# Kernel tuning notes

Hardware: AMD Instinct MI355X
Metric: run time of the kernel (lower is better)

Reference implementation:

```python
import jax, jax.numpy as jnp
import numpy as np

B = 16          # number of trees (batch)
H = 256         # hidden_size == feature_size
S = 16          # Tree.num_sem
C = 5           # max_child_num (complete C-ary tree)
L = 6           # tree depth: leaves at level L, internal levels 0..L-1
N_LEAF = C**L                     # 15625
N_INT = (C**L - 1) // (C - 1)     # 3906 internal nodes, level-l offset = (C^l-1)/(C-1)


def setup_inputs() -> dict:
    key = jax.random.key(0)
    ks = jax.random.split(key, 20)
    rn = lambda k, shp, s=0.05: jax.random.normal(k, shp, dtype=jnp.float32) * s
    return {
        "leaf_box": jax.random.normal(ks[0], (B, N_LEAF, 4), dtype=jnp.float32),
        "leaf_sem": jax.random.uniform(ks[1], (B, N_LEAF, S), dtype=jnp.float32),
        "internal_box": jax.random.normal(ks[2], (B, N_INT, 4), dtype=jnp.float32),
        "node_type": jax.random.randint(ks[3], (B, N_INT), 0, 3, dtype=jnp.int32),
        "eps": jax.random.normal(ks[4], (B, H), dtype=jnp.float32),
        "W_box": rn(ks[5], (4, H)), "b_box": jnp.zeros((H,), jnp.float32),
        "W_sem": rn(ks[6], (S, H)), "b_sem": jnp.zeros((H,), jnp.float32),
        "W_node": rn(ks[7], (3, C * H, H)), "b_node": jnp.zeros((3, H), jnp.float32),
        "W1": rn(ks[8], (H, H)), "b1": jnp.zeros((H,), jnp.float32),
        "Wmu": rn(ks[9], (H, H)), "bmu": jnp.zeros((H,), jnp.float32),
        "Wvar": rn(ks[10], (H, H)), "bvar": jnp.zeros((H,), jnp.float32),
    }


def reference(leaf_box, leaf_sem, internal_box, node_type, eps,
              W_box, b_box, W_sem, b_sem, W_node, b_node,
              W1, b1, Wmu, bmu, Wvar, bvar):
    box_enc = lambda b: jax.nn.relu(b @ W_box + b_box)
    # LeafEncoder: relu-box-encoding + relu-sem-encoding
    feats = box_enc(leaf_box) + jax.nn.relu(leaf_sem @ W_sem + b_sem)  # [B, N_LEAF, H]
    # Bottom-up over internal levels (static loop over L=6 levels)
    for l in range(L - 1, -1, -1):
        n = C ** l
        off = (C ** l - 1) // (C - 1)
        child = feats.reshape(B, n, C * H)  # children flattened per parent (child_exists==1)
        # Apply all 3 branch encoders (vertical/horizontal/stack), select by node label
        y_all = jnp.einsum('bnk,tkh->bnth', child, W_node) + b_node          # [B,n,3,H]
        sel = jax.nn.one_hot(node_type[:, off:off + n], 3, dtype=child.dtype)  # [B,n,3]
        y = jnp.einsum('bnth,bnt->bnh', y_all, sel)
        feats = jax.nn.relu(y) + box_enc(internal_box[:, off:off + n])
    root = feats[:, 0]  # [B, H]
    # Sampler (variational, probabilistic)
    enc = jax.nn.relu(root @ W1 + b1)
    mu = enc @ Wmu + bmu
    logvar = enc @ Wvar + bvar
    std = jnp.exp(0.5 * logvar)
    kld = 1.0 + logvar - mu ** 2 - jnp.exp(logvar)
    return jnp.concatenate([eps * std + mu, kld], axis=1)  # [B, 2H]
```

## Files before the change

kernel.cpp:

```cpp
#include <hip/hip_runtime.h>


#define B_ 16
#define H_ 256
#define NLEAF 15625
#define NINT 3906

typedef __bf16 bf16_t;
typedef bf16_t bf16x8 __attribute__((ext_vector_type(8)));
typedef bf16_t bf16x4 __attribute__((ext_vector_type(4)));
typedef float f32x4 __attribute__((ext_vector_type(4)));

__device__ __forceinline__ void gl2lds16(const bf16_t* g, bf16_t* l) {
  __builtin_amdgcn_global_load_lds((const __attribute__((address_space(1))) void*)g,
                                   (__attribute__((address_space(3))) void*)l,
                                   16, 0, 0);
}

__global__ __launch_bounds__(256) void prep_kernel(const float* __restrict__ W_node,
                                                   bf16_t* __restrict__ Wt,
                                                   int* __restrict__ counters) {
  if (blockIdx.x == 0 && threadIdx.x < 18) counters[threadIdx.x] = 0;
  const int t = blockIdx.x / 80;
  const int kc = blockIdx.x % 80;
  const int h = threadIdx.x;
  const float* srcp = W_node + (size_t)t * 1280 * 256 + h;
  bf16_t* dstp = Wt + ((size_t)(t * 256 + h)) * 1280;
#pragma unroll
  for (int k0 = kc * 16; k0 < kc * 16 + 16; k0 += 8) {
    bf16x8 v;
#pragma unroll
    for (int j = 0; j < 8; ++j) v[j] = (bf16_t)srcp[(size_t)(k0 + j) * 256];
    *(bf16x8*)(dstp + k0) = v;
  }
}

__global__ __launch_bounds__(256) void leaf_kernel(
    const float* __restrict__ leaf_box, const float* __restrict__ leaf_sem,
    const float* __restrict__ W_box, const float* __restrict__ b_box,
    const float* __restrict__ W_sem, const float* __restrict__ b_sem,
    bf16_t* __restrict__ f6) {
  const int lane = threadIdx.x & 63;
  const int wave = threadIdx.x >> 6;
  const int h0 = lane * 4;
  float wb[4][4], ws[16][4], bb[4], bs[4];
#pragma unroll
  for (int j = 0; j < 4; ++j) {
    float4 v = *(const float4*)(W_box + j * H_ + h0);
    wb[j][0] = v.x; wb[j][1] = v.y; wb[j][2] = v.z; wb[j][3] = v.w;
  }
#pragma unroll
  for (int j = 0; j < 16; ++j) {
    float4 v = *(const float4*)(W_sem + j * H_ + h0);
    ws[j][0] = v.x; ws[j][1] = v.y; ws[j][2] = v.z; ws[j][3] = v.w;
  }
  {
    float4 v = *(const float4*)(b_box + h0);
    bb[0] = v.x; bb[1] = v.y; bb[2] = v.z; bb[3] = v.w;
    float4 u = *(const float4*)(b_sem + h0);
    bs[0] = u.x; bs[1] = u.y; bs[2] = u.z; bs[3] = u.w;
  }
  const int ROWS = B_ * NLEAF;
  const int stride = gridDim.x * 4;
  for (int row = blockIdx.x * 4 + wave; row < ROWS; row += stride) {
    float4 bx = *(const float4*)(leaf_box + (size_t)row * 4);
    const float4* sp = (const float4*)(leaf_sem + (size_t)row * 16);
    float4 sv0 = sp[0], sv1 = sp[1], sv2 = sp[2], sv3 = sp[3];
    bf16x4 o;
#pragma unroll
    for (int c = 0; c < 4; ++c) {
      float s1 = fmaf(wb[0][c], bx.x, fmaf(wb[1][c], bx.y,
                 fmaf(wb[2][c], bx.z, fmaf(wb[3][c], bx.w, bb[c]))));
      float s2 = bs[c];
      s2 = fmaf(ws[0][c], sv0.x, s2);  s2 = fmaf(ws[1][c], sv0.y, s2);
      s2 = fmaf(ws[2][c], sv0.z, s2);  s2 = fmaf(ws[3][c], sv0.w, s2);
      s2 = fmaf(ws[4][c], sv1.x, s2);  s2 = fmaf(ws[5][c], sv1.y, s2);
      s2 = fmaf(ws[6][c], sv1.z, s2);  s2 = fmaf(ws[7][c], sv1.w, s2);
      s2 = fmaf(ws[8][c], sv2.x, s2);  s2 = fmaf(ws[9][c], sv2.y, s2);
      s2 = fmaf(ws[10][c], sv2.z, s2); s2 = fmaf(ws[11][c], sv2.w, s2);
      s2 = fmaf(ws[12][c], sv3.x, s2); s2 = fmaf(ws[13][c], sv3.y, s2);
      s2 = fmaf(ws[14][c], sv3.z, s2); s2 = fmaf(ws[15][c], sv3.w, s2);
      o[c] = (bf16_t)(fmaxf(s1, 0.f) + fmaxf(s2, 0.f));
    }
    *(bf16x4*)(f6 + (size_t)row * H_ + h0) = o;
  }
}

__global__ __launch_bounds__(256) void bucket_kernel(const int* __restrict__ node_type,
                                                     int* __restrict__ counters,
                                                     int2* __restrict__ buckets) {
  __shared__ int lcnt[18];
  __shared__ int lbase[18];
  const int tid = threadIdx.x;
  if (tid < 18) lcnt[tid] = 0;
  __syncthreads();

  int idx = blockIdx.x * 256 + tid;
  bool active = idx < B_ * NINT;
  int t = 0, key = 0, mypos = 0;
  int2 e;
  int base = 0, nl_cap = 0;
  if (active) {
    int b = idx / NINT;
    int j = idx - b * NINT;
    int l, off;
    if (j >= 781)      { l = 5; off = 781; }
    else if (j >= 156) { l = 4; off = 156; }
    else if (j >= 31)  { l = 3; off = 31; }
    else if (j >= 6)   { l = 2; off = 6; }
    else if (j >= 1)   { l = 1; off = 1; }
    else               { l = 0; off = 0; }
    const int n_tab[6]    = {1, 5, 25, 125, 625, 3125};
    const int nn_tab[6]   = {5, 25, 125, 625, 3125, 15625};
    const int base_tab[6] = {0, 48, 288, 1488, 7488, 37488};
    int n_l = n_tab[l], nn = nn_tab[l];
    t = node_type[idx];
    int i = j - off;
    e.x = b * n_l + i;
    e.y = b * nn + 5 * i;
    base = base_tab[l];
    nl_cap = B_ * n_l;
    key = l * 3 + t;
    mypos = atomicAdd(&lcnt[key], 1);
  }
  __syncthreads();
  if (tid < 18) {
    int c = lcnt[tid];
    lbase[tid] = c ? atomicAdd(&counters[tid], c) : 0;
  }
  __syncthreads();
  if (active) {
    buckets[base + t * nl_cap + lbase[key] + mypos] = e;
  }
}

__global__ __launch_bounds__(256) void level_kernel(
    const bf16_t* __restrict__ src, bf16_t* __restrict__ dst,
    const int2* __restrict__ bucket, const int* __restrict__ counters,
    const bf16_t* __restrict__ Wt, const float* __restrict__ b_node,
    const float* __restrict__ ibox, const float* __restrict__ W_box,
    const float* __restrict__ b_box, int n_l, int off_l, int cap) {
  const int t = blockIdx.y;
  const int cnt = counters[t];
  const int tile0 = blockIdx.x * 128;
  if (tile0 >= cnt) return;
  const int nblk = blockIdx.z;
  const int2* rd = bucket + (size_t)t * cap;

  __shared__ __align__(16) bf16_t Asm[2][128][64];
  __shared__ __align__(16) bf16_t Bsm[2][128][64];

  const int tid = threadIdx.x;
  const int lane = tid & 63;
  const int wave = tid >> 6;
  const int wm = wave & 1, wn = wave >> 1;
  const int quad = lane >> 4;
  const int l15 = lane & 15;

  const int r8 = tid >> 3;
  const int sc = tid & 7;
  const bf16_t* wsrc = Wt + ((size_t)t * 256 + nblk * 128) * 1280;
  const bf16_t* aptr[4];
  const bf16_t* bptr[4];
#pragma unroll
  for (int i = 0; i < 4; ++i) {
    int r = i * 32 + r8;
    int gch = sc ^ ((r >> 1) & 7);
    int ai = tile0 + r;
    if (ai >= cnt) ai = cnt - 1;
    aptr[i] = src + (size_t)rd[ai].y * H_ + gch * 8;
    bptr[i] = wsrc + (size_t)r * 1280 + gch * 8;
  }

  f32x4 acc[4][4];
#pragma unroll
  for (int i = 0; i < 4; ++i)
#pragma unroll
    for (int j = 0; j < 4; ++j) acc[i][j] = (f32x4){0.f, 0.f, 0.f, 0.f};

  const int sw = (l15 >> 1) & 7;
  const int pc0 = ((0 * 4 + quad) ^ sw) * 8;
  const int pc1 = ((1 * 4 + quad) ^ sw) * 8;

#define STAGE(buf, ks)                                          \
  {                                                             \
    const int ko = (ks) * 64;                                   \
    bf16_t* la = &Asm[buf][0][0] + wave * 512;                  \
    bf16_t* lb = &Bsm[buf][0][0] + wave * 512;                  \
    _Pragma("unroll") for (int i = 0; i < 4; ++i)               \
        gl2lds16(aptr[i] + ko, la + i * 2048);                  \
    _Pragma("unroll") for (int i = 0; i < 4; ++i)               \
        gl2lds16(bptr[i] + ko, lb + i * 2048);                  \
  }

  STAGE(0, 0)
  for (int ks = 0; ks < 20; ++ks) {
    const int buf = ks & 1;
    __syncthreads();
    bf16x8 af0[4], af1[4], bf0[4], bf1[4];
#pragma unroll
    for (int am = 0; am < 4; ++am) {
      af0[am] = *(const bf16x8*)(&Asm[buf][wm * 64 + am * 16 + l15][pc0]);
      af1[am] = *(const bf16x8*)(&Asm[buf][wm * 64 + am * 16 + l15][pc1]);
    }
#pragma unroll
    for (int bn = 0; bn < 4; ++bn) {
      bf0[bn] = *(const bf16x8*)(&Bsm[buf][wn * 64 + bn * 16 + l15][pc0]);
      bf1[bn] = *(const bf16x8*)(&Bsm[buf][wn * 64 + bn * 16 + l15][pc1]);
    }
    if (ks + 1 < 20) STAGE(buf ^ 1, ks + 1)
#pragma unroll
    for (int am = 0; am < 4; ++am)
#pragma unroll
      for (int bn = 0; bn < 4; ++bn)
        acc[am][bn] = __builtin_amdgcn_mfma_f32_16x16x32_bf16(af0[am], bf0[bn], acc[am][bn], 0, 0, 0);
#pragma unroll
    for (int am = 0; am < 4; ++am)
#pragma unroll
      for (int bn = 0; bn < 4; ++bn)
        acc[am][bn] = __builtin_amdgcn_mfma_f32_16x16x32_bf16(af1[am], bf1[bn], acc[am][bn], 0, 0, 0);
  }
#undef STAGE

  float wbv[4][6];
#pragma unroll
  for (int bn = 0; bn < 4; ++bn) {
    int col = nblk * 128 + wn * 64 + bn * 16 + l15;
    wbv[bn][0] = W_box[col];
    wbv[bn][1] = W_box[H_ + col];
    wbv[bn][2] = W_box[2 * H_ + col];
    wbv[bn][3] = W_box[3 * H_ + col];
    wbv[bn][4] = b_box[col];
    wbv[bn][5] = b_node[t * H_ + col];
  }
#pragma unroll
  for (int am = 0; am < 4; ++am) {
    int orow[4]; float4 bxv[4]; bool valid[4];
#pragma unroll
    for (int r = 0; r < 4; ++r) {
      int gidx = tile0 + wm * 64 + am * 16 + quad * 4 + r;
      valid[r] = (gidx < cnt);
      int ic = valid[r] ? gidx : (cnt - 1);
      int orw = rd[ic].x;
      orow[r] = orw;
      int b = orw / n_l;
      int i = orw - b * n_l;
      bxv[r] = *(const float4*)(ibox + ((size_t)b * NINT + off_l + i) * 4);
    }
#pragma unroll
    for (int bn = 0; bn < 4; ++bn) {
      int col = nblk * 128 + wn * 64 + bn * 16 + l15;
#pragma unroll
      for (int r = 0; r < 4; ++r) {
        if (!valid[r]) continue;
        float y = fmaxf(acc[am][bn][r] + wbv[bn][5], 0.f);
        float be = fmaf(wbv[bn][0], bxv[r].x,
                   fmaf(wbv[bn][1], bxv[r].y,
                   fmaf(wbv[bn][2], bxv[r].z,
                   fmaf(wbv[bn][3], bxv[r].w, wbv[bn][4]))));
        be = fmaxf(be, 0.f);
        dst[(size_t)orow[r] * H_ + col] = (bf16_t)(y + be);
      }
    }
  }
}

__global__ __launch_bounds__(256) void head_kernel(
    const bf16_t* __restrict__ f0, const float* __restrict__ eps,
    const float* __restrict__ W1, const float* __restrict__ b1,
    const float* __restrict__ Wmu, const float* __restrict__ bmu,
    const float* __restrict__ Wvar, const float* __restrict__ bvar,
    float* __restrict__ out) {
  __shared__ float root[256];
  __shared__ float enc[256];
  int b = blockIdx.x, h = threadIdx.x;
  root[h] = (float)f0[b * H_ + h];
  __syncthreads();
  float a = b1[h];
  for (int k = 0; k < 256; ++k) a = fmaf(root[k], W1[k * H_ + h], a);
  enc[h] = fmaxf(a, 0.f);
  __syncthreads();
  float m = bmu[h], lv = bvar[h];
  for (int k = 0; k < 256; ++k) {
    float e = enc[k];
    m = fmaf(e, Wmu[k * H_ + h], m);
    lv = fmaf(e, Wvar[k * H_ + h], lv);
  }
  float stdv = expf(0.5f * lv);
  float kld = 1.f + lv - m * m - expf(lv);
  out[b * 512 + h] = eps[b * H_ + h] * stdv + m;
  out[b * 512 + 256 + h] = kld;
}

extern "C" void kernel_launch(void* const* d_in, const int* in_sizes, int n_in,
                              void* d_out, int out_size, void* d_ws, size_t ws_size,
                              hipStream_t stream) {
  const float* leaf_box     = (const float*)d_in[0];
  const float* leaf_sem     = (const float*)d_in[1];
  const float* internal_box = (const float*)d_in[2];
  const int*   node_type    = (const int*)d_in[3];
  const float* eps          = (const float*)d_in[4];
  const float* W_box        = (const float*)d_in[5];
  const float* b_box        = (const float*)d_in[6];
  const float* W_sem        = (const float*)d_in[7];
  const float* b_sem        = (const float*)d_in[8];
  const float* W_node       = (const float*)d_in[9];
  const float* b_node       = (const float*)d_in[10];
  const float* W1           = (const float*)d_in[11];
  const float* b1           = (const float*)d_in[12];
  const float* Wmu          = (const float*)d_in[13];
  const float* bmu          = (const float*)d_in[14];
  const float* Wvar         = (const float*)d_in[15];
  const float* bvar         = (const float*)d_in[16];
  float* out = (float*)d_out;

  char* p = (char*)d_ws;
  auto alloc = [&](size_t bytes) {
    char* r = p;
    p += (bytes + 255) & ~(size_t)255;
    return r;
  };
  bf16_t* Wt = (bf16_t*)alloc((size_t)3 * 256 * 1280 * 2);
  const int n_tab[7] = {1, 5, 25, 125, 625, 3125, 15625};
  bf16_t* f[7];
  for (int l = 0; l <= 6; ++l) f[l] = (bf16_t*)alloc((size_t)B_ * n_tab[l] * H_ * 2);
  int* counters = (int*)alloc(18 * 4);
  int2* buckets = (int2*)alloc((size_t)187488 * 8);

  hipLaunchKernelGGL(prep_kernel, dim3(240), dim3(256), 0, stream, W_node, Wt, counters);
  hipLaunchKernelGGL(leaf_kernel, dim3(2048), dim3(256), 0, stream,
                     leaf_box, leaf_sem, W_box, b_box, W_sem, b_sem, f[6]);
  hipLaunchKernelGGL(bucket_kernel, dim3((B_ * NINT + 255) / 256), dim3(256), 0, stream,
                     node_type, counters, buckets);

  const int lvl_base[6] = {0, 48, 288, 1488, 7488, 37488};
  const int off_tab[6]  = {0, 1, 6, 31, 156, 781};
  for (int l = 5; l >= 0; --l) {
    int cap = B_ * n_tab[l];
    int tiles = (cap + 127) / 128;
    hipLaunchKernelGGL(level_kernel, dim3(tiles, 3, 2), dim3(256), 0, stream,
                       f[l + 1], f[l], buckets + lvl_base[l], counters + l * 3,
                       Wt, b_node, internal_box, W_box, b_box,
                       n_tab[l], off_tab[l], cap);
  }
  hipLaunchKernelGGL(head_kernel, dim3(16), dim3(256), 0, stream,
                     f[0], eps, W1, b1, Wmu, bmu, Wvar, bvar, out);
}
```

Measured before the change: 392.7 us.

## Scatter node features directly into type-sorted contiguous GEMM input rows

Producers (leaf kernel and each level kernel) now compute each parent's position in the type-bucketed order and write child features straight into a contiguous A matrix of 1280-wide rows. The level GEMM then reads its A operand as plain contiguous rows instead of gathering through bucket indices. This removes the indirect gather on the A loads and makes them fully sequential. In exchange the writes become scattered, and extra node_pos/node_type lookups are added in the epilogues. The head kernel also gets an unroll pragma.

```diff
diff --git a/kernel.cpp b/kernel.cpp
--- a/kernel.cpp
+++ b/kernel.cpp
@@ -35,60 +35,10 @@
   }
 }
 
-__global__ __launch_bounds__(256) void leaf_kernel(
-    const float* __restrict__ leaf_box, const float* __restrict__ leaf_sem,
-    const float* __restrict__ W_box, const float* __restrict__ b_box,
-    const float* __restrict__ W_sem, const float* __restrict__ b_sem,
-    bf16_t* __restrict__ f6) {
-  const int lane = threadIdx.x & 63;
-  const int wave = threadIdx.x >> 6;
-  const int h0 = lane * 4;
-  float wb[4][4], ws[16][4], bb[4], bs[4];
-#pragma unroll
-  for (int j = 0; j < 4; ++j) {
-    float4 v = *(const float4*)(W_box + j * H_ + h0);
-    wb[j][0] = v.x; wb[j][1] = v.y; wb[j][2] = v.z; wb[j][3] = v.w;
-  }
-#pragma unroll
-  for (int j = 0; j < 16; ++j) {
-    float4 v = *(const float4*)(W_sem + j * H_ + h0);
-    ws[j][0] = v.x; ws[j][1] = v.y; ws[j][2] = v.z; ws[j][3] = v.w;
-  }
-  {
-    float4 v = *(const float4*)(b_box + h0);
-    bb[0] = v.x; bb[1] = v.y; bb[2] = v.z; bb[3] = v.w;
-    float4 u = *(const float4*)(b_sem + h0);
-    bs[0] = u.x; bs[1] = u.y; bs[2] = u.z; bs[3] = u.w;
-  }
-  const int ROWS = B_ * NLEAF;
-  const int stride = gridDim.x * 4;
-  for (int row = blockIdx.x * 4 + wave; row < ROWS; row += stride) {
-    float4 bx = *(const float4*)(leaf_box + (size_t)row * 4);
-    const float4* sp = (const float4*)(leaf_sem + (size_t)row * 16);
-    float4 sv0 = sp[0], sv1 = sp[1], sv2 = sp[2], sv3 = sp[3];
-    bf16x4 o;
-#pragma unroll
-    for (int c = 0; c < 4; ++c) {
-      float s1 = fmaf(wb[0][c], bx.x, fmaf(wb[1][c], bx.y,
-                 fmaf(wb[2][c], bx.z, fmaf(wb[3][c], bx.w, bb[c]))));
-      float s2 = bs[c];
-      s2 = fmaf(ws[0][c], sv0.x, s2);  s2 = fmaf(ws[1][c], sv0.y, s2);
-      s2 = fmaf(ws[2][c], sv0.z, s2);  s2 = fmaf(ws[3][c], sv0.w, s2);
-      s2 = fmaf(ws[4][c], sv1.x, s2);  s2 = fmaf(ws[5][c], sv1.y, s2);
-      s2 = fmaf(ws[6][c], sv1.z, s2);  s2 = fmaf(ws[7][c], sv1.w, s2);
-      s2 = fmaf(ws[8][c], sv2.x, s2);  s2 = fmaf(ws[9][c], sv2.y, s2);
-      s2 = fmaf(ws[10][c], sv2.z, s2); s2 = fmaf(ws[11][c], sv2.w, s2);
-      s2 = fmaf(ws[12][c], sv3.x, s2); s2 = fmaf(ws[13][c], sv3.y, s2);
-      s2 = fmaf(ws[14][c], sv3.z, s2); s2 = fmaf(ws[15][c], sv3.w, s2);
-      o[c] = (bf16_t)(fmaxf(s1, 0.f) + fmaxf(s2, 0.f));
-    }
-    *(bf16x4*)(f6 + (size_t)row * H_ + h0) = o;
-  }
-}
-
 __global__ __launch_bounds__(256) void bucket_kernel(const int* __restrict__ node_type,
                                                      int* __restrict__ counters,
-                                                     int2* __restrict__ buckets) {
+                                                     int2* __restrict__ buckets,
+                                                     int* __restrict__ node_pos) {
   __shared__ int lcnt[18];
   __shared__ int lbase[18];
   const int tid = threadIdx.x;
@@ -110,14 +60,14 @@
     else if (j >= 6)   { l = 2; off = 6; }
     else if (j >= 1)   { l = 1; off = 1; }
     else               { l = 0; off = 0; }
-    const int n_tab[6]    = {1, 5, 25, 125, 625, 3125};
-    const int nn_tab[6]   = {5, 25, 125, 625, 3125, 15625};
-    const int base_tab[6] = {0, 48, 288, 1488, 7488, 37488};
-    int n_l = n_tab[l], nn = nn_tab[l];
+    const int n_tab[6]        = {1, 5, 25, 125, 625, 3125};
+    const int base_tab[6]     = {0, 48, 288, 1488, 7488, 37488};
+    const int off_prev_tab[6] = {0, 0, 1, 6, 31, 156};
+    int n_l = n_tab[l];
     t = node_type[idx];
     int i = j - off;
     e.x = b * n_l + i;
-    e.y = b * nn + 5 * i;
+    e.y = (l == 0) ? b : (b * NINT + off_prev_tab[l] + i / 5);
     base = base_tab[l];
     nl_cap = B_ * n_l;
     key = l * 3 + t;
@@ -130,20 +80,88 @@
   }
   __syncthreads();
   if (active) {
-    buckets[base + t * nl_cap + lbase[key] + mypos] = e;
+    int pos = lbase[key] + mypos;
+    buckets[base + t * nl_cap + pos] = e;
+    node_pos[idx] = pos;
+  }
+}
+
+__global__ __launch_bounds__(256) void leaf_kernel(
+    const float* __restrict__ leaf_box, const float* __restrict__ leaf_sem,
+    const float* __restrict__ W_box, const float* __restrict__ b_box,
+    const float* __restrict__ W_sem, const float* __restrict__ b_sem,
+    const int* __restrict__ node_type, const int* __restrict__ node_pos,
+    const int* __restrict__ counters5, bf16_t* __restrict__ A5) {
+  const int lane = threadIdx.x & 63;
+  const int wave = threadIdx.x >> 6;
+  const int h0 = lane * 4;
+  float wb[4][4], ws[16][4], bb[4], bs[4];
+#pragma unroll
+  for (int j = 0; j < 4; ++j) {
+    float4 v = *(const float4*)(W_box + j * H_ + h0);
+    wb[j][0] = v.x; wb[j][1] = v.y; wb[j][2] = v.z; wb[j][3] = v.w;
+  }
+#pragma unroll
+  for (int j = 0; j < 16; ++j) {
+    float4 v = *(const float4*)(W_sem + j * H_ + h0);
+    ws[j][0] = v.x; ws[j][1] = v.y; ws[j][2] = v.z; ws[j][3] = v.w;
+  }
+  {
+    float4 v = *(const float4*)(b_box + h0);
+    bb[0] = v.x; bb[1] = v.y; bb[2] = v.z; bb[3] = v.w;
+    float4 u = *(const float4*)(b_sem + h0);
+    bs[0] = u.x; bs[1] = u.y; bs[2] = u.z; bs[3] = u.w;
+  }
+  const int c15 = counters5[0], c16 = counters5[1];
+  const int GROUPS = B_ * 3125;
+  const int stride = gridDim.x * 4;
+  for (int g = blockIdx.x * 4 + wave; g < GROUPS; g += stride) {
+    int b = g / 3125;
+    int i = g - b * 3125;
+    int pidx = b * NINT + 781 + i;
+    int pt = node_type[pidx];
+    int gpos = node_pos[pidx] + (pt > 0 ? c15 : 0) + (pt > 1 ? c16 : 0);
+    size_t outbase = (size_t)gpos * 1280 + h0;
+    size_t leaf0 = (size_t)b * NLEAF + 5 * i;
+#pragma unroll
+    for (int c = 0; c < 5; ++c) {
+      float4 bx = *(const float4*)(leaf_box + (leaf0 + c) * 4);
+      const float4* sp = (const float4*)(leaf_sem + (leaf0 + c) * 16);
+      float4 sv0 = sp[0], sv1 = sp[1], sv2 = sp[2], sv3 = sp[3];
+      bf16x4 o;
+#pragma unroll
+      for (int ch = 0; ch < 4; ++ch) {
+        float s1 = fmaf(wb[0][ch], bx.x, fmaf(wb[1][ch], bx.y,
+                   fmaf(wb[2][ch], bx.z, fmaf(wb[3][ch], bx.w, bb[ch]))));
+        float s2 = bs[ch];
+        s2 = fmaf(ws[0][ch], sv0.x, s2);  s2 = fmaf(ws[1][ch], sv0.y, s2);
+        s2 = fmaf(ws[2][ch], sv0.z, s2);  s2 = fmaf(ws[3][ch], sv0.w, s2);
+        s2 = fmaf(ws[4][ch], sv1.x, s2);  s2 = fmaf(ws[5][ch], sv1.y, s2);
+        s2 = fmaf(ws[6][ch], sv1.z, s2);  s2 = fmaf(ws[7][ch], sv1.w, s2);
+        s2 = fmaf(ws[8][ch], sv2.x, s2);  s2 = fmaf(ws[9][ch], sv2.y, s2);
+        s2 = fmaf(ws[10][ch], sv2.z, s2); s2 = fmaf(ws[11][ch], sv2.w, s2);
+        s2 = fmaf(ws[12][ch], sv3.x, s2); s2 = fmaf(ws[13][ch], sv3.y, s2);
+        s2 = fmaf(ws[14][ch], sv3.z, s2); s2 = fmaf(ws[15][ch], sv3.w, s2);
+        o[ch] = (bf16_t)(fmaxf(s1, 0.f) + fmaxf(s2, 0.f));
+      }
+      *(bf16x4*)(A5 + outbase + c * 256) = o;
+    }
   }
 }
 
 __global__ __launch_bounds__(256) void level_kernel(
-    const bf16_t* __restrict__ src, bf16_t* __restrict__ dst,
+    const bf16_t* __restrict__ Ain, bf16_t* __restrict__ Aout,
     const int2* __restrict__ bucket, const int* __restrict__ counters,
+    const int* __restrict__ pcounters, const int* __restrict__ node_pos,
+    const int* __restrict__ node_type,
     const bf16_t* __restrict__ Wt, const float* __restrict__ b_node,
     const float* __restrict__ ibox, const float* __restrict__ W_box,
-    const float* __restrict__ b_box, int n_l, int off_l, int cap) {
+    const float* __restrict__ b_box, int n_l, int off_l, int cap, int is_root) {
   const int t = blockIdx.y;
   const int cnt = counters[t];
   const int tile0 = blockIdx.x * 128;
   if (tile0 >= cnt) return;
+  const int tbase = (t > 0 ? counters[0] : 0) + (t > 1 ? counters[1] : 0);
   const int nblk = blockIdx.z;
   const int2* rd = bucket + (size_t)t * cap;
 
@@ -166,9 +184,7 @@
   for (int i = 0; i < 4; ++i) {
     int r = i * 32 + r8;
     int gch = sc ^ ((r >> 1) & 7);
-    int ai = tile0 + r;
-    if (ai >= cnt) ai = cnt - 1;
-    aptr[i] = src + (size_t)rd[ai].y * H_ + gch * 8;
+    aptr[i] = Ain + (size_t)(tbase + tile0 + r) * 1280 + gch * 8;
     bptr[i] = wsrc + (size_t)r * 1280 + gch * 8;
   }
 
@@ -222,6 +238,7 @@
   }
 #undef STAGE
 
+  const int pc0v = pcounters[0], pc1v = pcounters[1];
   float wbv[4][6];
 #pragma unroll
   for (int bn = 0; bn < 4; ++bn) {
@@ -235,17 +252,28 @@
   }
 #pragma unroll
   for (int am = 0; am < 4; ++am) {
-    int orow[4]; float4 bxv[4]; bool valid[4];
+    size_t wofs[4]; float4 bxv[4]; bool valid[4];
 #pragma unroll
     for (int r = 0; r < 4; ++r) {
       int gidx = tile0 + wm * 64 + am * 16 + quad * 4 + r;
       valid[r] = (gidx < cnt);
       int ic = valid[r] ? gidx : (cnt - 1);
-      int orw = rd[ic].x;
-      orow[r] = orw;
-      int b = orw / n_l;
-      int i = orw - b * n_l;
+      int2 e = rd[ic];
+      int orow = e.x;
+      int b = orow / n_l;
+      int i = orow - b * n_l;
       bxv[r] = *(const float4*)(ibox + ((size_t)b * NINT + off_l + i) * 4);
+      int wtgt;
+      if (is_root) {
+        wtgt = orow;
+      } else {
+        int pidx = e.y;
+        int pt = node_type[pidx];
+        int gpos = node_pos[pidx] + (pt > 0 ? pc0v : 0) + (pt > 1 ? pc1v : 0);
+        int cs = i - (i / 5) * 5;
+        wtgt = gpos * 5 + cs;
+      }
+      wofs[r] = (size_t)wtgt * 256;
     }
 #pragma unroll
     for (int bn = 0; bn < 4; ++bn) {
@@ -259,7 +287,7 @@
                    fmaf(wbv[bn][2], bxv[r].z,
                    fmaf(wbv[bn][3], bxv[r].w, wbv[bn][4]))));
         be = fmaxf(be, 0.f);
-        dst[(size_t)orow[r] * H_ + col] = (bf16_t)(y + be);
+        Aout[wofs[r] + col] = (bf16_t)(y + be);
       }
     }
   }
@@ -277,10 +305,12 @@
   root[h] = (float)f0[b * H_ + h];
   __syncthreads();
   float a = b1[h];
+#pragma unroll 8
   for (int k = 0; k < 256; ++k) a = fmaf(root[k], W1[k * H_ + h], a);
   enc[h] = fmaxf(a, 0.f);
   __syncthreads();
   float m = bmu[h], lv = bvar[h];
+#pragma unroll 8
   for (int k = 0; k < 256; ++k) {
     float e = enc[k];
     m = fmaf(e, Wmu[k * H_ + h], m);
@@ -321,28 +351,35 @@
     return r;
   };
   bf16_t* Wt = (bf16_t*)alloc((size_t)3 * 256 * 1280 * 2);
-  const int n_tab[7] = {1, 5, 25, 125, 625, 3125, 15625};
-  bf16_t* f[7];
-  for (int l = 0; l <= 6; ++l) f[l] = (bf16_t*)alloc((size_t)B_ * n_tab[l] * H_ * 2);
+  const int n_nodes[6] = {1, 5, 25, 125, 625, 3125};
+  bf16_t* A[6];
+  for (int l = 0; l < 6; ++l)
+    A[l] = (bf16_t*)alloc(((size_t)B_ * n_nodes[l] + 128) * 1280 * 2);
+  bf16_t* f0 = (bf16_t*)alloc((size_t)B_ * H_ * 2);
   int* counters = (int*)alloc(18 * 4);
+  int* node_pos = (int*)alloc((size_t)B_ * NINT * 4);
   int2* buckets = (int2*)alloc((size_t)187488 * 8);
 
   hipLaunchKernelGGL(prep_kernel, dim3(240), dim3(256), 0, stream, W_node, Wt, counters);
+  hipLaunchKernelGGL(bucket_kernel, dim3((B_ * NINT + 255) / 256), dim3(256), 0, stream,
+                     node_type, counters, buckets, node_pos);
   hipLaunchKernelGGL(leaf_kernel, dim3(2048), dim3(256), 0, stream,
-                     leaf_box, leaf_sem, W_box, b_box, W_sem, b_sem, f[6]);
-  hipLaunchKernelGGL(bucket_kernel, dim3((B_ * NINT + 255) / 256), dim3(256), 0, stream,
-                     node_type, counters, buckets);
+                     leaf_box, leaf_sem, W_box, b_box, W_sem, b_sem,
+                     node_type, node_pos, counters + 15, A[5]);
 
   const int lvl_base[6] = {0, 48, 288, 1488, 7488, 37488};
   const int off_tab[6]  = {0, 1, 6, 31, 156, 781};
   for (int l = 5; l >= 0; --l) {
-    int cap = B_ * n_tab[l];
+    int cap = B_ * n_nodes[l];
     int tiles = (cap + 127) / 128;
+    bf16_t* Aout = (l > 0) ? A[l - 1] : f0;
+    const int* pctr = (l > 0) ? (counters + (l - 1) * 3) : counters;
     hipLaunchKernelGGL(level_kernel, dim3(tiles, 3, 2), dim3(256), 0, stream,
-                       f[l + 1], f[l], buckets + lvl_base[l], counters + l * 3,
+                       A[l], Aout, buckets + lvl_base[l], counters + l * 3, pctr,
+                       node_pos, node_type,
                        Wt, b_node, internal_box, W_box, b_box,
-                       n_tab[l], off_tab[l], cap);
+                       n_nodes[l], off_tab[l], cap, (l == 0) ? 1 : 0);
   }
   hipLaunchKernelGGL(head_kernel, dim3(16), dim3(256), 0, stream,
-                     f[0], eps, W1, b1, Wmu, bmu, Wvar, bvar, out);
-}
+                     f0, eps, W1, b1, Wmu, bmu, Wvar, bvar, out);
+}
```

Measured after the change: 438.8 us. 11.7% more time.

## Fuse upper tree levels and head into one persistent kernel with grid barriers

Applied to the files above, without the earlier changes.

Merges weight prep and bucketing into one launch, keeps level 5 as its own kernel, and runs levels 4..0 plus the VAE head in a single persistent 256-block kernel with atomic grid barriers between levels. It also unrolls the leaf kernel to four rows per wave. The goal is to remove the launch overhead and tail latency of the small upper levels, at the cost of spin-wait barriers that need all 256 blocks to be resident at once, and idle blocks on the tiny levels.

```diff
diff --git a/kernel.cpp b/kernel.cpp
--- a/kernel.cpp
+++ b/kernel.cpp
@@ -5,6 +5,7 @@
 #define H_ 256
 #define NLEAF 15625
 #define NINT 3906
+#define GPERS 256
 
 typedef __bf16 bf16_t;
 typedef bf16_t bf16x8 __attribute__((ext_vector_type(8)));
@@ -17,85 +18,30 @@
                                    16, 0, 0);
 }
 
-__global__ __launch_bounds__(256) void prep_kernel(const float* __restrict__ W_node,
-                                                   bf16_t* __restrict__ Wt,
-                                                   int* __restrict__ counters) {
-  if (blockIdx.x == 0 && threadIdx.x < 18) counters[threadIdx.x] = 0;
-  const int t = blockIdx.x / 80;
-  const int kc = blockIdx.x % 80;
-  const int h = threadIdx.x;
-  const float* srcp = W_node + (size_t)t * 1280 * 256 + h;
-  bf16_t* dstp = Wt + ((size_t)(t * 256 + h)) * 1280;
-#pragma unroll
-  for (int k0 = kc * 16; k0 < kc * 16 + 16; k0 += 8) {
-    bf16x8 v;
-#pragma unroll
-    for (int j = 0; j < 8; ++j) v[j] = (bf16_t)srcp[(size_t)(k0 + j) * 256];
-    *(bf16x8*)(dstp + k0) = v;
-  }
-}
-
-__global__ __launch_bounds__(256) void leaf_kernel(
-    const float* __restrict__ leaf_box, const float* __restrict__ leaf_sem,
-    const float* __restrict__ W_box, const float* __restrict__ b_box,
-    const float* __restrict__ W_sem, const float* __restrict__ b_sem,
-    bf16_t* __restrict__ f6) {
-  const int lane = threadIdx.x & 63;
-  const int wave = threadIdx.x >> 6;
-  const int h0 = lane * 4;
-  float wb[4][4], ws[16][4], bb[4], bs[4];
-#pragma unroll
-  for (int j = 0; j < 4; ++j) {
-    float4 v = *(const float4*)(W_box + j * H_ + h0);
-    wb[j][0] = v.x; wb[j][1] = v.y; wb[j][2] = v.z; wb[j][3] = v.w;
-  }
-#pragma unroll
-  for (int j = 0; j < 16; ++j) {
-    float4 v = *(const float4*)(W_sem + j * H_ + h0);
-    ws[j][0] = v.x; ws[j][1] = v.y; ws[j][2] = v.z; ws[j][3] = v.w;
-  }
-  {
-    float4 v = *(const float4*)(b_box + h0);
-    bb[0] = v.x; bb[1] = v.y; bb[2] = v.z; bb[3] = v.w;
-    float4 u = *(const float4*)(b_sem + h0);
-    bs[0] = u.x; bs[1] = u.y; bs[2] = u.z; bs[3] = u.w;
-  }
-  const int ROWS = B_ * NLEAF;
-  const int stride = gridDim.x * 4;
-  for (int row = blockIdx.x * 4 + wave; row < ROWS; row += stride) {
-    float4 bx = *(const float4*)(leaf_box + (size_t)row * 4);
-    const float4* sp = (const float4*)(leaf_sem + (size_t)row * 16);
-    float4 sv0 = sp[0], sv1 = sp[1], sv2 = sp[2], sv3 = sp[3];
-    bf16x4 o;
-#pragma unroll
-    for (int c = 0; c < 4; ++c) {
-      float s1 = fmaf(wb[0][c], bx.x, fmaf(wb[1][c], bx.y,
-                 fmaf(wb[2][c], bx.z, fmaf(wb[3][c], bx.w, bb[c]))));
-      float s2 = bs[c];
-      s2 = fmaf(ws[0][c], sv0.x, s2);  s2 = fmaf(ws[1][c], sv0.y, s2);
-      s2 = fmaf(ws[2][c], sv0.z, s2);  s2 = fmaf(ws[3][c], sv0.w, s2);
-      s2 = fmaf(ws[4][c], sv1.x, s2);  s2 = fmaf(ws[5][c], sv1.y, s2);
-      s2 = fmaf(ws[6][c], sv1.z, s2);  s2 = fmaf(ws[7][c], sv1.w, s2);
-      s2 = fmaf(ws[8][c], sv2.x, s2);  s2 = fmaf(ws[9][c], sv2.y, s2);
-      s2 = fmaf(ws[10][c], sv2.z, s2); s2 = fmaf(ws[11][c], sv2.w, s2);
-      s2 = fmaf(ws[12][c], sv3.x, s2); s2 = fmaf(ws[13][c], sv3.y, s2);
-      s2 = fmaf(ws[14][c], sv3.z, s2); s2 = fmaf(ws[15][c], sv3.w, s2);
-      o[c] = (bf16_t)(fmaxf(s1, 0.f) + fmaxf(s2, 0.f));
-    }
-    *(bf16x4*)(f6 + (size_t)row * H_ + h0) = o;
-  }
-}
-
-__global__ __launch_bounds__(256) void bucket_kernel(const int* __restrict__ node_type,
-                                                     int* __restrict__ counters,
-                                                     int2* __restrict__ buckets) {
+__global__ __launch_bounds__(256) void prep_bucket_kernel(
+    const float* __restrict__ W_node, bf16_t* __restrict__ Wt,
+    const int* __restrict__ node_type, int* __restrict__ counters,
+    int2* __restrict__ buckets) {
+  const int tid = threadIdx.x;
+  if (blockIdx.x < 240) {
+    const int t = blockIdx.x / 80;
+    const int kc = blockIdx.x % 80;
+    const float* srcp = W_node + (size_t)t * 1280 * 256 + tid;
+    bf16_t* dstp = Wt + ((size_t)(t * 256 + tid)) * 1280;
+#pragma unroll
+    for (int k0 = kc * 16; k0 < kc * 16 + 16; k0 += 8) {
+      bf16x8 v;
+#pragma unroll
+      for (int j = 0; j < 8; ++j) v[j] = (bf16_t)srcp[(size_t)(k0 + j) * 256];
+      *(bf16x8*)(dstp + k0) = v;
+    }
+    return;
+  }
   __shared__ int lcnt[18];
   __shared__ int lbase[18];
-  const int tid = threadIdx.x;
   if (tid < 18) lcnt[tid] = 0;
   __syncthreads();
-
-  int idx = blockIdx.x * 256 + tid;
+  int idx = (blockIdx.x - 240) * 256 + tid;
   bool active = idx < B_ * NINT;
   int t = 0, key = 0, mypos = 0;
   int2 e;
@@ -129,27 +75,73 @@
     lbase[tid] = c ? atomicAdd(&counters[tid], c) : 0;
   }
   __syncthreads();
-  if (active) {
-    buckets[base + t * nl_cap + lbase[key] + mypos] = e;
-  }
-}
-
-__global__ __launch_bounds__(256) void level_kernel(
+  if (active) buckets[base + t * nl_cap + lbase[key] + mypos] = e;
+}
+
+__global__ __launch_bounds__(256) void leaf_kernel(
+    const float* __restrict__ leaf_box, const float* __restrict__ leaf_sem,
+    const float* __restrict__ W_box, const float* __restrict__ b_box,
+    const float* __restrict__ W_sem, const float* __restrict__ b_sem,
+    bf16_t* __restrict__ f6) {
+  const int lane = threadIdx.x & 63;
+  const int wave = threadIdx.x >> 6;
+  const int h0 = lane * 4;
+  float wb[4][4], ws[16][4], bb[4], bs[4];
+#pragma unroll
+  for (int j = 0; j < 4; ++j) {
+    float4 v = *(const float4*)(W_box + j * H_ + h0);
+    wb[j][0] = v.x; wb[j][1] = v.y; wb[j][2] = v.z; wb[j][3] = v.w;
+  }
+#pragma unroll
+  for (int j = 0; j < 16; ++j) {
+    float4 v = *(const float4*)(W_sem + j * H_ + h0);
+    ws[j][0] = v.x; ws[j][1] = v.y; ws[j][2] = v.z; ws[j][3] = v.w;
+  }
+  {
+    float4 v = *(const float4*)(b_box + h0);
+    bb[0] = v.x; bb[1] = v.y; bb[2] = v.z; bb[3] = v.w;
+    float4 u = *(const float4*)(b_sem + h0);
+    bs[0] = u.x; bs[1] = u.y; bs[2] = u.z; bs[3] = u.w;
+  }
+  const int ROWS = B_ * NLEAF;
+  const int stride = gridDim.x * 16;
+  for (int row = blockIdx.x * 16 + wave * 4; row < ROWS; row += stride) {
+    float4 bx[4]; float4 sv[4][4];
+#pragma unroll
+    for (int r = 0; r < 4; ++r) {
+      bx[r] = *(const float4*)(leaf_box + (size_t)(row + r) * 4);
+      const float4* sp = (const float4*)(leaf_sem + (size_t)(row + r) * 16);
+      sv[r][0] = sp[0]; sv[r][1] = sp[1]; sv[r][2] = sp[2]; sv[r][3] = sp[3];
+    }
+#pragma unroll
+    for (int r = 0; r < 4; ++r) {
+      bf16x4 o;
+#pragma unroll
+      for (int c = 0; c < 4; ++c) {
+        float s1 = fmaf(wb[0][c], bx[r].x, fmaf(wb[1][c], bx[r].y,
+                   fmaf(wb[2][c], bx[r].z, fmaf(wb[3][c], bx[r].w, bb[c]))));
+        float s2 = bs[c];
+#pragma unroll
+        for (int j = 0; j < 4; ++j) {
+          s2 = fmaf(ws[4*j+0][c], sv[r][j].x, s2);
+          s2 = fmaf(ws[4*j+1][c], sv[r][j].y, s2);
+          s2 = fmaf(ws[4*j+2][c], sv[r][j].z, s2);
+          s2 = fmaf(ws[4*j+3][c], sv[r][j].w, s2);
+        }
+        o[c] = (bf16_t)(fmaxf(s1, 0.f) + fmaxf(s2, 0.f));
+      }
+      *(bf16x4*)(f6 + (size_t)(row + r) * H_ + h0) = o;
+    }
+  }
+}
+
+__device__ __forceinline__ void level_tile(
+    bf16_t* __restrict__ As, bf16_t* __restrict__ Bs,
     const bf16_t* __restrict__ src, bf16_t* __restrict__ dst,
-    const int2* __restrict__ bucket, const int* __restrict__ counters,
-    const bf16_t* __restrict__ Wt, const float* __restrict__ b_node,
+    const int2* __restrict__ rd, int cnt,
+    const bf16_t* __restrict__ wsrc, const float* __restrict__ b_node_t,
     const float* __restrict__ ibox, const float* __restrict__ W_box,
-    const float* __restrict__ b_box, int n_l, int off_l, int cap) {
-  const int t = blockIdx.y;
-  const int cnt = counters[t];
-  const int tile0 = blockIdx.x * 128;
-  if (tile0 >= cnt) return;
-  const int nblk = blockIdx.z;
-  const int2* rd = bucket + (size_t)t * cap;
-
-  __shared__ __align__(16) bf16_t Asm[2][128][64];
-  __shared__ __align__(16) bf16_t Bsm[2][128][64];
-
+    const float* __restrict__ b_box, int n_l, int off_l, int tile0, int nblk) {
   const int tid = threadIdx.x;
   const int lane = tid & 63;
   const int wave = tid >> 6;
@@ -159,7 +151,6 @@
 
   const int r8 = tid >> 3;
   const int sc = tid & 7;
-  const bf16_t* wsrc = Wt + ((size_t)t * 256 + nblk * 128) * 1280;
   const bf16_t* aptr[4];
   const bf16_t* bptr[4];
 #pragma unroll
@@ -179,18 +170,18 @@
     for (int j = 0; j < 4; ++j) acc[i][j] = (f32x4){0.f, 0.f, 0.f, 0.f};
 
   const int sw = (l15 >> 1) & 7;
-  const int pc0 = ((0 * 4 + quad) ^ sw) * 8;
-  const int pc1 = ((1 * 4 + quad) ^ sw) * 8;
-
-#define STAGE(buf, ks)                                          \
-  {                                                             \
-    const int ko = (ks) * 64;                                   \
-    bf16_t* la = &Asm[buf][0][0] + wave * 512;                  \
-    bf16_t* lb = &Bsm[buf][0][0] + wave * 512;                  \
-    _Pragma("unroll") for (int i = 0; i < 4; ++i)               \
-        gl2lds16(aptr[i] + ko, la + i * 2048);                  \
-    _Pragma("unroll") for (int i = 0; i < 4; ++i)               \
-        gl2lds16(bptr[i] + ko, lb + i * 2048);                  \
+  const int pc0 = (quad ^ sw) * 8;
+  const int pc1 = ((4 + quad) ^ sw) * 8;
+
+#define STAGE(buf, ks)                                            \
+  {                                                               \
+    const int ko = (ks) * 64;                                     \
+    bf16_t* la = As + (buf) * 8192 + wave * 512;                  \
+    bf16_t* lb = Bs + (buf) * 8192 + wave * 512;                  \
+    _Pragma("unroll") for (int i = 0; i < 4; ++i)                 \
+        gl2lds16(aptr[i] + ko, la + i * 2048);                    \
+    _Pragma("unroll") for (int i = 0; i < 4; ++i)                 \
+        gl2lds16(bptr[i] + ko, lb + i * 2048);                    \
   }
 
   STAGE(0, 0)
@@ -200,13 +191,15 @@
     bf16x8 af0[4], af1[4], bf0[4], bf1[4];
 #pragma unroll
     for (int am = 0; am < 4; ++am) {
-      af0[am] = *(const bf16x8*)(&Asm[buf][wm * 64 + am * 16 + l15][pc0]);
-      af1[am] = *(const bf16x8*)(&Asm[buf][wm * 64 + am * 16 + l15][pc1]);
+      const bf16_t* rp = As + buf * 8192 + (wm * 64 + am * 16 + l15) * 64;
+      af0[am] = *(const bf16x8*)(rp + pc0);
+      af1[am] = *(const bf16x8*)(rp + pc1);
     }
 #pragma unroll
     for (int bn = 0; bn < 4; ++bn) {
-      bf0[bn] = *(const bf16x8*)(&Bsm[buf][wn * 64 + bn * 16 + l15][pc0]);
-      bf1[bn] = *(const bf16x8*)(&Bsm[buf][wn * 64 + bn * 16 + l15][pc1]);
+      const bf16_t* rp = Bs + buf * 8192 + (wn * 64 + bn * 16 + l15) * 64;
+      bf0[bn] = *(const bf16x8*)(rp + pc0);
+      bf1[bn] = *(const bf16x8*)(rp + pc1);
     }
     if (ks + 1 < 20) STAGE(buf ^ 1, ks + 1)
 #pragma unroll
@@ -221,6 +214,7 @@
         acc[am][bn] = __builtin_amdgcn_mfma_f32_16x16x32_bf16(af1[am], bf1[bn], acc[am][bn], 0, 0, 0);
   }
 #undef STAGE
+  __syncthreads();
 
   float wbv[4][6];
 #pragma unroll
@@ -231,7 +225,7 @@
     wbv[bn][2] = W_box[2 * H_ + col];
     wbv[bn][3] = W_box[3 * H_ + col];
     wbv[bn][4] = b_box[col];
-    wbv[bn][5] = b_node[t * H_ + col];
+    wbv[bn][5] = b_node_t[col];
   }
 #pragma unroll
   for (int am = 0; am < 4; ++am) {
@@ -265,22 +259,95 @@
   }
 }
 
-__global__ __launch_bounds__(256) void head_kernel(
-    const bf16_t* __restrict__ f0, const float* __restrict__ eps,
-    const float* __restrict__ W1, const float* __restrict__ b1,
-    const float* __restrict__ Wmu, const float* __restrict__ bmu,
-    const float* __restrict__ Wvar, const float* __restrict__ bvar,
-    float* __restrict__ out) {
+__global__ __launch_bounds__(256) void level5_kernel(
+    const bf16_t* __restrict__ src, bf16_t* __restrict__ dst,
+    const int2* __restrict__ bucket, const int* __restrict__ counters,
+    const bf16_t* __restrict__ Wt, const float* __restrict__ b_node,
+    const float* __restrict__ ibox, const float* __restrict__ W_box,
+    const float* __restrict__ b_box) {
+  __shared__ __align__(16) bf16_t As[2 * 128 * 64];
+  __shared__ __align__(16) bf16_t Bs[2 * 128 * 64];
+  const int t = blockIdx.y;
+  const int cnt = counters[15 + t];
+  const int tile0 = blockIdx.x * 128;
+  if (tile0 >= cnt) return;
+  const int nblk = blockIdx.z;
+  level_tile(As, Bs, src, dst, bucket + 37488 + (size_t)t * (B_ * 3125), cnt,
+             Wt + ((size_t)t * 256 + nblk * 128) * 1280, b_node + t * H_,
+             ibox, W_box, b_box, 3125, 781, tile0, nblk);
+}
+
+__device__ __forceinline__ void gbar(int* ctr) {
+  __syncthreads();
+  if (threadIdx.x == 0) {
+    __threadfence();
+    atomicAdd(ctr, 1);
+    while (__hip_atomic_load(ctr, __ATOMIC_ACQUIRE, __HIP_MEMORY_SCOPE_AGENT) < GPERS)
+      __builtin_amdgcn_s_sleep(1);
+    __threadfence();
+  }
+  __syncthreads();
+}
+
+__global__ __launch_bounds__(256) void fused_kernel(
+    const bf16_t* __restrict__ f5, bf16_t* __restrict__ f4,
+    bf16_t* __restrict__ f3, bf16_t* __restrict__ f2,
+    bf16_t* __restrict__ f1, bf16_t* __restrict__ f0,
+    const int2* __restrict__ buckets, const int* __restrict__ counters,
+    int* __restrict__ bars,
+    const bf16_t* __restrict__ Wt, const float* __restrict__ b_node,
+    const float* __restrict__ ibox, const float* __restrict__ W_box,
+    const float* __restrict__ b_box,
+    const float* __restrict__ eps, const float* __restrict__ W1,
+    const float* __restrict__ b1, const float* __restrict__ Wmu,
+    const float* __restrict__ bmu, const float* __restrict__ Wvar,
+    const float* __restrict__ bvar, float* __restrict__ out) {
+  __shared__ __align__(16) bf16_t As[2 * 128 * 64];
+  __shared__ __align__(16) bf16_t Bs[2 * 128 * 64];
+
+  const bf16_t* fin[5]  = {f5, f4, f3, f2, f1};
+  bf16_t* fout[5]       = {f4, f3, f2, f1, f0};
+  const int nl_tab[5]   = {625, 125, 25, 5, 1};
+  const int off_tab[5]  = {156, 31, 6, 1, 0};
+  const int base_tab[5] = {7488, 1488, 288, 48, 0};
+
+#pragma unroll 1
+  for (int li = 0; li < 5; ++li) {
+    const int l = 4 - li;
+    const int c0 = counters[l * 3 + 0];
+    const int c1 = counters[l * 3 + 1];
+    const int c2 = counters[l * 3 + 2];
+    const int T0 = (c0 + 127) >> 7, T1 = (c1 + 127) >> 7, T2 = (c2 + 127) >> 7;
+    const int W = 2 * (T0 + T1 + T2);
+    const int cap = B_ * nl_tab[li];
+#pragma unroll 1
+    for (int w = blockIdx.x; w < W; w += GPERS) {
+      int nblk = w & 1, q = w >> 1;
+      int t, tile, cnt;
+      if (q < T0)           { t = 0; tile = q;           cnt = c0; }
+      else if (q < T0 + T1) { t = 1; tile = q - T0;      cnt = c1; }
+      else                  { t = 2; tile = q - T0 - T1; cnt = c2; }
+      level_tile(As, Bs, fin[li], fout[li],
+                 buckets + base_tab[li] + (size_t)t * cap, cnt,
+                 Wt + ((size_t)t * 256 + nblk * 128) * 1280, b_node + t * H_,
+                 ibox, W_box, b_box, nl_tab[li], off_tab[li], tile * 128, nblk);
+    }
+    gbar(bars + li);
+  }
+
+  if (blockIdx.x >= B_) return;
   __shared__ float root[256];
   __shared__ float enc[256];
   int b = blockIdx.x, h = threadIdx.x;
   root[h] = (float)f0[b * H_ + h];
   __syncthreads();
   float a = b1[h];
+#pragma unroll 8
   for (int k = 0; k < 256; ++k) a = fmaf(root[k], W1[k * H_ + h], a);
   enc[h] = fmaxf(a, 0.f);
   __syncthreads();
   float m = bmu[h], lv = bvar[h];
+#pragma unroll 8
   for (int k = 0; k < 256; ++k) {
     float e = enc[k];
     m = fmaf(e, Wmu[k * H_ + h], m);
@@ -324,25 +391,21 @@
   const int n_tab[7] = {1, 5, 25, 125, 625, 3125, 15625};
   bf16_t* f[7];
   for (int l = 0; l <= 6; ++l) f[l] = (bf16_t*)alloc((size_t)B_ * n_tab[l] * H_ * 2);
-  int* counters = (int*)alloc(18 * 4);
+  int* counters = (int*)alloc(24 * 4);
+  int* bars = counters + 18;
   int2* buckets = (int2*)alloc((size_t)187488 * 8);
 
-  hipLaunchKernelGGL(prep_kernel, dim3(240), dim3(256), 0, stream, W_node, Wt, counters);
+  hipMemsetAsync(counters, 0, 24 * 4, stream);
+  hipLaunchKernelGGL(prep_bucket_kernel, dim3(485), dim3(256), 0, stream,
+                     W_node, Wt, node_type, counters, buckets);
   hipLaunchKernelGGL(leaf_kernel, dim3(2048), dim3(256), 0, stream,
                      leaf_box, leaf_sem, W_box, b_box, W_sem, b_sem, f[6]);
-  hipLaunchKernelGGL(bucket_kernel, dim3((B_ * NINT + 255) / 256), dim3(256), 0, stream,
-                     node_type, counters, buckets);
-
-  const int lvl_base[6] = {0, 48, 288, 1488, 7488, 37488};
-  const int off_tab[6]  = {0, 1, 6, 31, 156, 781};
-  for (int l = 5; l >= 0; --l) {
-    int cap = B_ * n_tab[l];
-    int tiles = (cap + 127) / 128;
-    hipLaunchKernelGGL(level_kernel, dim3(tiles, 3, 2), dim3(256), 0, stream,
-                       f[l + 1], f[l], buckets + lvl_base[l], counters + l * 3,
-                       Wt, b_node, internal_box, W_box, b_box,
-                       n_tab[l], off_tab[l], cap);
-  }
-  hipLaunchKernelGGL(head_kernel, dim3(16), dim3(256), 0, stream,
-                     f[0], eps, W1, b1, Wmu, bmu, Wvar, bvar, out);
-}
+  hipLaunchKernelGGL(level5_kernel, dim3(391, 3, 2), dim3(256), 0, stream,
+                     f[6], f[5], buckets, counters, Wt, b_node,
+                     internal_box, W_box, b_box);
+  hipLaunchKernelGGL(fused_kernel, dim3(GPERS), dim3(256), 0, stream,
+                     f[5], f[4], f[3], f[2], f[1], f[0],
+                     buckets, counters, bars, Wt, b_node,
+                     internal_box, W_box, b_box,
+                     eps, W1, b1, Wmu, bmu, Wvar, bvar, out);
+}
```

Result: slower. 935.0 us (+138.1%).
